# Kernel optimization log

Measured on AMD Instinct MI355X. Metric: run time of the kernel, lower is better.

## Reference

```python
import jax, jax.numpy as jnp
import numpy as np

E = 2_000_000   # edges
N = 200_000     # nodes
E_DIM = 128     # edge feature dim
G_DIM = 256     # global/graph feature dim
B = 1024        # number of graphs (batch.max()+1)
EPS = 1e-6      # torch_scatter scatter_std eps


def setup_inputs() -> dict:
    key = jax.random.key(0)
    k1, k2, k3, k4 = jax.random.split(key, 4)
    e = jax.random.normal(k1, (E, E_DIM), dtype=jnp.float32)
    e_index = jax.random.randint(k2, (2, E), 0, N, dtype=jnp.int64)
    batch = jnp.sort(jax.random.randint(k3, (N,), 0, B, dtype=jnp.int64))
    fc_w = jax.random.normal(k4, (E_DIM * 4, G_DIM), dtype=jnp.float32) * 0.02
    fc_b = jnp.zeros((G_DIM,), dtype=jnp.float32)
    return {"e_index": e_index, "e": e, "batch": batch, "fc_w": fc_w, "fc_b": fc_b}


def reference(e_index, e, batch, fc_w, fc_b):
    # graph id per edge (via target node of each edge)
    e_batch = batch[e_index[1]]  # [E]

    count = jax.ops.segment_sum(jnp.ones((e.shape[0],), e.dtype), e_batch,
                                num_segments=B)[:, None]  # [B, 1]
    s = jax.ops.segment_sum(e, e_batch, num_segments=B)    # [B, D]

    # scatter(reduce='mean'): empty segments -> 0 (divide by clamped count)
    mean = s / jnp.maximum(count, 1.0)

    # scatter min/max: torch_scatter fills empty segments with 0
    mn = jax.ops.segment_min(e, e_batch, num_segments=B)
    mx = jax.ops.segment_max(e, e_batch, num_segments=B)
    empty = count == 0.0
    mn = jnp.where(empty, 0.0, mn)
    mx = jnp.where(empty, 0.0, mx)

    # scatter_std (unbiased, matches torch_scatter composite):
    # std = sqrt(sum((x - mean)^2) / (clamp(count-1, 1) + eps))
    diff = e - mean[e_batch]                               # [E, D]
    var_sum = jax.ops.segment_sum(diff * diff, e_batch, num_segments=B)
    denom = jnp.maximum(count - 1.0, 1.0) + EPS
    std = jnp.sqrt(var_sum / denom)

    g = jnp.concatenate([mean, mn, mx, std], axis=1)       # [B, 4D]
    return g @ fc_w + fc_b                                 # [B, G_DIM]
```

## Files before the change

### kernel.cpp

```cpp
#include <hip/hip_runtime.h>
#include <math.h>

#define DIMS 128
#define GD 256
#define MAXB 1024
#define NSLOT 8
#define NBLK 256
#define SCH 8192

typedef float vfloat4 __attribute__((ext_vector_type(4)));

__device__ __forceinline__ float4 ldnt(const float* p) {
    vfloat4 v = __builtin_nontemporal_load(reinterpret_cast<const vfloat4*>(p));
    return make_float4(v.x, v.y, v.z, v.w);
}
__device__ __forceinline__ float4 f4_add(float4 a, float4 b) {
    return make_float4(a.x + b.x, a.y + b.y, a.z + b.z, a.w + b.w);
}
__device__ __forceinline__ float4 f4_min(float4 a, float4 b) {
    return make_float4(fminf(a.x, b.x), fminf(a.y, b.y), fminf(a.z, b.z), fminf(a.w, b.w));
}
__device__ __forceinline__ float4 f4_max(float4 a, float4 b) {
    return make_float4(fmaxf(a.x, b.x), fmaxf(a.y, b.y), fmaxf(a.z, b.z), fmaxf(a.w, b.w));
}

#define ACC(v) do { \
    sm = f4_add(sm, v); \
    sq = f4_add(sq, make_float4((v).x*(v).x, (v).y*(v).y, (v).z*(v).z, (v).w*(v).w)); \
    mn = f4_min(mn, v); mx = f4_max(mx, v); } while (0)

__global__ void __launch_bounds__(256)
hist2_kernel(const int* __restrict__ e_index, const int* __restrict__ batch,
             int E, int* __restrict__ hist2r, unsigned short* __restrict__ eb) {
    __shared__ int lh[MAXB];
    for (int i = threadIdx.x; i < MAXB; i += 256) lh[i] = 0;
    __syncthreads();
    int b = blockIdx.x;
    int CH = (E + NBLK - 1) / NBLK;
    int lo = b * CH;
    int hi = min(E, lo + CH);
    for (int j = lo + threadIdx.x; j < hi; j += 256) {
        int node = e_index[E + j];
        int g = batch[node];
        eb[j] = (unsigned short)g;
        atomicAdd(&lh[g], 1);
    }
    __syncthreads();
    for (int i = threadIdx.x; i < MAXB; i += 256)
        hist2r[(size_t)b * MAXB + i] = lh[i];
}

__global__ void __launch_bounds__(256)
colscan_kernel(const int* __restrict__ hist2r, int* __restrict__ hist2s,
               int* __restrict__ count) {
    int g = blockIdx.x;
    int t = threadIdx.x;
    int v = hist2r[(size_t)t * MAXB + g];
    __shared__ int ws[256];
    ws[t] = v;
    __syncthreads();
    for (int d = 1; d < 256; d <<= 1) {
        int x = (t >= d) ? ws[t - d] : 0;
        __syncthreads();
        ws[t] += x;
        __syncthreads();
    }
    hist2s[(size_t)t * MAXB + g] = ws[t] - v;
    if (t == 255) count[g] = ws[255];
}

__global__ void __launch_bounds__(256)
scatter_kernel(const unsigned short* __restrict__ eb, const int* __restrict__ hist2r,
               const int* __restrict__ hist2s, const int* __restrict__ count, int E,
               int* __restrict__ perm, int* __restrict__ offs) {
    __shared__ int lofs[MAXB];
    __shared__ int lcur[MAXB];
    __shared__ int lbase[MAXB];
    __shared__ int ws[256];
    __shared__ int bin[SCH];
    int b = blockIdx.x;
    int t = threadIdx.x;
    int CH = (E + NBLK - 1) / NBLK;
    int lo = b * CH;
    int hi = min(E, lo + CH);
    int base = t * 4;

    int g0 = count[base + 0], g1 = count[base + 1], g2 = count[base + 2], g3 = count[base + 3];
    int gsum = g0 + g1 + g2 + g3;
    ws[t] = gsum;
    __syncthreads();
    for (int d = 1; d < 256; d <<= 1) {
        int x = (t >= d) ? ws[t - d] : 0;
        __syncthreads();
        ws[t] += x;
        __syncthreads();
    }
    int gexcl = ws[t] - gsum;
    int ob0 = gexcl, ob1 = gexcl + g0, ob2 = gexcl + g0 + g1, ob3 = gexcl + g0 + g1 + g2;
    if (b == 0) {
        offs[base + 0] = ob0; offs[base + 1] = ob1;
        offs[base + 2] = ob2; offs[base + 3] = ob3;
    }
    lbase[base + 0] = ob0 + hist2s[(size_t)b * MAXB + base + 0];
    lbase[base + 1] = ob1 + hist2s[(size_t)b * MAXB + base + 1];
    lbase[base + 2] = ob2 + hist2s[(size_t)b * MAXB + base + 2];
    lbase[base + 3] = ob3 + hist2s[(size_t)b * MAXB + base + 3];
    __syncthreads();

    int c0 = hist2r[(size_t)b * MAXB + base + 0];
    int c1 = hist2r[(size_t)b * MAXB + base + 1];
    int c2 = hist2r[(size_t)b * MAXB + base + 2];
    int c3 = hist2r[(size_t)b * MAXB + base + 3];
    int s0 = c0 + c1 + c2 + c3;
    ws[t] = s0;
    __syncthreads();
    for (int d = 1; d < 256; d <<= 1) {
        int x = (t >= d) ? ws[t - d] : 0;
        __syncthreads();
        ws[t] += x;
        __syncthreads();
    }
    int excl = ws[t] - s0;
    lofs[base + 0] = excl;
    lofs[base + 1] = excl + c0;
    lofs[base + 2] = excl + c0 + c1;
    lofs[base + 3] = excl + c0 + c1 + c2;
    lcur[base + 0] = excl;
    lcur[base + 1] = excl + c0;
    lcur[base + 2] = excl + c0 + c1;
    lcur[base + 3] = excl + c0 + c1 + c2;
    __syncthreads();

    for (int j = lo + t; j < hi; j += 256) {
        int g = eb[j];
        int r = atomicAdd(&lcur[g], 1);
        bin[r] = j;
    }
    __syncthreads();

    int grp = t >> 3, sub = t & 7;
    for (int g = grp; g < MAXB; g += 32) {
        int sfrom = lofs[g];
        int n = lcur[g] - sfrom;
        int dst = lbase[g];
        for (int k = sub; k < n; k += 8)
            perm[dst + k] = bin[sfrom + k];
    }
}

__global__ void __launch_bounds__(256)
reduce_kernel(const float* __restrict__ e, const int* __restrict__ perm,
              const int* __restrict__ offs, const int* __restrict__ count,
              float* __restrict__ gbuf) {
    int g = blockIdx.x;
    int start = offs[g];
    int cnt = count[g];
    const int* pp = perm + start;

    int c = threadIdx.x & 31;
    int s = threadIdx.x >> 5;

    float4 sm = make_float4(0.f, 0.f, 0.f, 0.f);
    float4 sq = make_float4(0.f, 0.f, 0.f, 0.f);
    float4 mn = make_float4(INFINITY, INFINITY, INFINITY, INFINITY);
    float4 mx = make_float4(-INFINITY, -INFINITY, -INFINITY, -INFINITY);

    int i = s;
    if (i + 3 * NSLOT < cnt) {
        int ia0 = pp[i], ia1 = pp[i + NSLOT], ia2 = pp[i + 2 * NSLOT], ia3 = pp[i + 3 * NSLOT];
        while (true) {
            int ni = i + 4 * NSLOT;
            int na0 = 0, na1 = 0, na2 = 0, na3 = 0;
            bool nok = (ni + 3 * NSLOT < cnt);
            if (nok) { na0 = pp[ni]; na1 = pp[ni + NSLOT]; na2 = pp[ni + 2 * NSLOT]; na3 = pp[ni + 3 * NSLOT]; }
            float4 v0 = ldnt(e + (size_t)ia0 * DIMS + c * 4);
            float4 v1 = ldnt(e + (size_t)ia1 * DIMS + c * 4);
            float4 v2 = ldnt(e + (size_t)ia2 * DIMS + c * 4);
            float4 v3 = ldnt(e + (size_t)ia3 * DIMS + c * 4);
            ACC(v0); ACC(v1); ACC(v2); ACC(v3);
            i = ni;
            if (!nok) break;
            ia0 = na0; ia1 = na1; ia2 = na2; ia3 = na3;
        }
    }
    for (; i < cnt; i += NSLOT) {
        int r = pp[i];
        float4 v = ldnt(e + (size_t)r * DIMS + c * 4);
        ACC(v);
    }

    __shared__ float4 red[4][NSLOT][32];
    red[0][s][c] = sm;
    red[1][s][c] = mn;
    red[2][s][c] = mx;
    red[3][s][c] = sq;
    __syncthreads();

    int t = threadIdx.x;
    if (t < 128) {
        int stat = t >> 5;
        int cc = t & 31;
        float4 a = red[stat][0][cc];
        if (stat == 1) {
#pragma unroll
            for (int k = 1; k < NSLOT; ++k) a = f4_min(a, red[1][k][cc]);
        } else if (stat == 2) {
#pragma unroll
            for (int k = 1; k < NSLOT; ++k) a = f4_max(a, red[2][k][cc]);
        } else {
#pragma unroll
            for (int k = 1; k < NSLOT; ++k) a = f4_add(a, red[stat][k][cc]);
        }
        float fc = (float)cnt;
        float fcm = fmaxf(fc, 1.0f);
        float4 r;
        if (stat == 0) {
            r = make_float4(a.x / fcm, a.y / fcm, a.z / fcm, a.w / fcm);
        } else if (stat == 1 || stat == 2) {
            r = (cnt == 0) ? make_float4(0.f, 0.f, 0.f, 0.f) : a;
        } else {
            float4 smr = red[0][0][cc];
#pragma unroll
            for (int k = 1; k < NSLOT; ++k) smr = f4_add(smr, red[0][k][cc]);
            float4 mean = make_float4(smr.x / fcm, smr.y / fcm, smr.z / fcm, smr.w / fcm);
            float denom = fmaxf(fc - 1.0f, 1.0f) + 1e-6f;
            r = make_float4(sqrtf(fmaxf(a.x - smr.x * mean.x, 0.f) / denom),
                            sqrtf(fmaxf(a.y - smr.y * mean.y, 0.f) / denom),
                            sqrtf(fmaxf(a.z - smr.z * mean.z, 0.f) / denom),
                            sqrtf(fmaxf(a.w - smr.w * mean.w, 0.f) / denom));
        }
        *reinterpret_cast<float4*>(gbuf + (size_t)g * 512 + stat * DIMS + cc * 4) = r;
    }
}

__global__ void __launch_bounds__(256)
gemm_kernel(const float* __restrict__ gbuf, const float* __restrict__ w,
            const float* __restrict__ bias, float* __restrict__ out, int B) {
    __shared__ float gl[8 * 512];
    int r0 = blockIdx.x * 8;
    int t = threadIdx.x;
    for (int i = t; i < 8 * 512; i += 256) {
        int r = r0 + (i >> 9);
        gl[i] = (r < B) ? gbuf[(size_t)r0 * 512 + i] : 0.f;
    }
    __syncthreads();

    int col = t;
    float acc[8];
    float bv = bias[col];
#pragma unroll
    for (int r = 0; r < 8; ++r) acc[r] = bv;
#pragma unroll 4
    for (int k = 0; k < 512; ++k) {
        float wv = w[k * GD + col];
#pragma unroll
        for (int r = 0; r < 8; ++r) acc[r] += gl[r * 512 + k] * wv;
    }
#pragma unroll
    for (int r = 0; r < 8; ++r) {
        int rr = r0 + r;
        if (rr < B) out[(size_t)rr * GD + col] = acc[r];
    }
}

extern "C" void kernel_launch(void* const* d_in, const int* in_sizes, int n_in,
                              void* d_out, int out_size, void* d_ws, size_t ws_size,
                              hipStream_t stream) {
    const int*   e_index = (const int*)d_in[0];
    const float* e       = (const float*)d_in[1];
    const int*   batch   = (const int*)d_in[2];
    const float* fc_w    = (const float*)d_in[3];
    const float* fc_b    = (const float*)d_in[4];
    float* out = (float*)d_out;

    int E = in_sizes[1] / DIMS;
    int B = out_size / GD;

    int* hist2r = (int*)d_ws;
    int* hist2s = hist2r + (size_t)NBLK * MAXB;
    int* count  = hist2s + (size_t)NBLK * MAXB;
    int* offs   = count + MAXB;
    unsigned short* eb = (unsigned short*)(offs + MAXB);
    int* perm   = (int*)(eb + (((size_t)E + 1) & ~(size_t)1));
    float* gbuf = (float*)(perm + E);

    hist2_kernel<<<NBLK, 256, 0, stream>>>(e_index, batch, E, hist2r, eb);
    colscan_kernel<<<MAXB, 256, 0, stream>>>(hist2r, hist2s, count);
    scatter_kernel<<<NBLK, 256, 0, stream>>>(eb, hist2r, hist2s, count, E, perm, offs);
    reduce_kernel<<<MAXB, 256, 0, stream>>>(e, perm, offs, count, gbuf);
    gemm_kernel<<<(B + 7) / 8, 256, 0, stream>>>(gbuf, fc_w, fc_b, out, B);
}
```

Measured before the change: 262.5 us.

## Fuse histogram/scan/scatter into cooperative kernel and split reduce per graph

Merges the histogram, column scan and scatter kernels into one cooperative kernel that uses grid.sync, removing two launches and their gaps. The reduce kernel now runs two blocks per graph, each handling half the edges and writing partial sum/min/max/sumsq. The GEMM kernel combines the two partials and finalizes mean/min/max/std before the matmul. This doubles reduce parallelism to better saturate memory bandwidth, at the cost of grid-wide barriers and a larger partial buffer.

Result: slower. 344.9 us (+31.4%).

```diff
diff --git a/kernel.cpp b/kernel.cpp
--- a/kernel.cpp
+++ b/kernel.cpp
@@ -1,10 +1,14 @@
 #include <hip/hip_runtime.h>
+#include <hip/hip_cooperative_groups.h>
 #include <math.h>
+
+namespace cg = cooperative_groups;
 
 #define DIMS 128
 #define GD 256
 #define MAXB 1024
 #define NSLOT 8
+#define PARTS 2
 #define NBLK 256
 #define SCH 8192
 
@@ -30,54 +34,17 @@
     mn = f4_min(mn, v); mx = f4_max(mx, v); } while (0)
 
 __global__ void __launch_bounds__(256)
-hist2_kernel(const int* __restrict__ e_index, const int* __restrict__ batch,
-             int E, int* __restrict__ hist2r, unsigned short* __restrict__ eb) {
+prep_kernel(const int* __restrict__ e_index, const int* __restrict__ batch, int E,
+            int* __restrict__ hist2r, int* __restrict__ hist2s,
+            int* __restrict__ count, int* __restrict__ offs,
+            unsigned short* __restrict__ eb, int* __restrict__ perm) {
     __shared__ int lh[MAXB];
-    for (int i = threadIdx.x; i < MAXB; i += 256) lh[i] = 0;
-    __syncthreads();
-    int b = blockIdx.x;
-    int CH = (E + NBLK - 1) / NBLK;
-    int lo = b * CH;
-    int hi = min(E, lo + CH);
-    for (int j = lo + threadIdx.x; j < hi; j += 256) {
-        int node = e_index[E + j];
-        int g = batch[node];
-        eb[j] = (unsigned short)g;
-        atomicAdd(&lh[g], 1);
-    }
-    __syncthreads();
-    for (int i = threadIdx.x; i < MAXB; i += 256)
-        hist2r[(size_t)b * MAXB + i] = lh[i];
-}
-
-__global__ void __launch_bounds__(256)
-colscan_kernel(const int* __restrict__ hist2r, int* __restrict__ hist2s,
-               int* __restrict__ count) {
-    int g = blockIdx.x;
-    int t = threadIdx.x;
-    int v = hist2r[(size_t)t * MAXB + g];
     __shared__ int ws[256];
-    ws[t] = v;
-    __syncthreads();
-    for (int d = 1; d < 256; d <<= 1) {
-        int x = (t >= d) ? ws[t - d] : 0;
-        __syncthreads();
-        ws[t] += x;
-        __syncthreads();
-    }
-    hist2s[(size_t)t * MAXB + g] = ws[t] - v;
-    if (t == 255) count[g] = ws[255];
-}
-
-__global__ void __launch_bounds__(256)
-scatter_kernel(const unsigned short* __restrict__ eb, const int* __restrict__ hist2r,
-               const int* __restrict__ hist2s, const int* __restrict__ count, int E,
-               int* __restrict__ perm, int* __restrict__ offs) {
-    __shared__ int lofs[MAXB];
     __shared__ int lcur[MAXB];
     __shared__ int lbase[MAXB];
-    __shared__ int ws[256];
     __shared__ int bin[SCH];
+
+    cg::grid_group grid = cg::this_grid();
     int b = blockIdx.x;
     int t = threadIdx.x;
     int CH = (E + NBLK - 1) / NBLK;
@@ -85,6 +52,38 @@
     int hi = min(E, lo + CH);
     int base = t * 4;
 
+    for (int i = t; i < MAXB; i += 256) lh[i] = 0;
+    __syncthreads();
+    for (int j = lo + t; j < hi; j += 256) {
+        int node = e_index[E + j];
+        int g = batch[node];
+        eb[j] = (unsigned short)g;
+        atomicAdd(&lh[g], 1);
+    }
+    __syncthreads();
+    for (int i = t; i < MAXB; i += 256)
+        hist2r[(size_t)b * MAXB + i] = lh[i];
+
+    grid.sync();
+
+    for (int q = 0; q < 4; ++q) {
+        int g = b * 4 + q;
+        int v = hist2r[(size_t)t * MAXB + g];
+        ws[t] = v;
+        __syncthreads();
+        for (int d = 1; d < 256; d <<= 1) {
+            int x = (t >= d) ? ws[t - d] : 0;
+            __syncthreads();
+            ws[t] += x;
+            __syncthreads();
+        }
+        hist2s[(size_t)t * MAXB + g] = ws[t] - v;
+        if (t == 255) count[g] = ws[255];
+        __syncthreads();
+    }
+
+    grid.sync();
+
     int g0 = count[base + 0], g1 = count[base + 1], g2 = count[base + 2], g3 = count[base + 3];
     int gsum = g0 + g1 + g2 + g3;
     ws[t] = gsum;
@@ -121,10 +120,10 @@
         __syncthreads();
     }
     int excl = ws[t] - s0;
-    lofs[base + 0] = excl;
-    lofs[base + 1] = excl + c0;
-    lofs[base + 2] = excl + c0 + c1;
-    lofs[base + 3] = excl + c0 + c1 + c2;
+    lh[base + 0] = excl;
+    lh[base + 1] = excl + c0;
+    lh[base + 2] = excl + c0 + c1;
+    lh[base + 3] = excl + c0 + c1 + c2;
     lcur[base + 0] = excl;
     lcur[base + 1] = excl + c0;
     lcur[base + 2] = excl + c0 + c1;
@@ -140,7 +139,7 @@
 
     int grp = t >> 3, sub = t & 7;
     for (int g = grp; g < MAXB; g += 32) {
-        int sfrom = lofs[g];
+        int sfrom = lh[g];
         int n = lcur[g] - sfrom;
         int dst = lbase[g];
         for (int k = sub; k < n; k += 8)
@@ -151,11 +150,18 @@
 __global__ void __launch_bounds__(256)
 reduce_kernel(const float* __restrict__ e, const int* __restrict__ perm,
               const int* __restrict__ offs, const int* __restrict__ count,
-              float* __restrict__ gbuf) {
-    int g = blockIdx.x;
+              float* __restrict__ pbuf) {
+    int bid = blockIdx.x;
+    int g = bid >> 1;
+    int p = bid & 1;
     int start = offs[g];
     int cnt = count[g];
-    const int* pp = perm + start;
+    int chunk = (cnt + PARTS - 1) / PARTS;
+    int bb = p * chunk;
+    int cnt_p = cnt - bb;
+    if (cnt_p > chunk) cnt_p = chunk;
+    if (cnt_p < 0) cnt_p = 0;
+    const int* pp = perm + start + bb;
 
     int c = threadIdx.x & 31;
     int s = threadIdx.x >> 5;
@@ -166,12 +172,12 @@
     float4 mx = make_float4(-INFINITY, -INFINITY, -INFINITY, -INFINITY);
 
     int i = s;
-    if (i + 3 * NSLOT < cnt) {
+    if (i + 3 * NSLOT < cnt_p) {
         int ia0 = pp[i], ia1 = pp[i + NSLOT], ia2 = pp[i + 2 * NSLOT], ia3 = pp[i + 3 * NSLOT];
         while (true) {
             int ni = i + 4 * NSLOT;
             int na0 = 0, na1 = 0, na2 = 0, na3 = 0;
-            bool nok = (ni + 3 * NSLOT < cnt);
+            bool nok = (ni + 3 * NSLOT < cnt_p);
             if (nok) { na0 = pp[ni]; na1 = pp[ni + NSLOT]; na2 = pp[ni + 2 * NSLOT]; na3 = pp[ni + 3 * NSLOT]; }
             float4 v0 = ldnt(e + (size_t)ia0 * DIMS + c * 4);
             float4 v1 = ldnt(e + (size_t)ia1 * DIMS + c * 4);
@@ -183,7 +189,7 @@
             ia0 = na0; ia1 = na1; ia2 = na2; ia3 = na3;
         }
     }
-    for (; i < cnt; i += NSLOT) {
+    for (; i < cnt_p; i += NSLOT) {
         int r = pp[i];
         float4 v = ldnt(e + (size_t)r * DIMS + c * 4);
         ACC(v);
@@ -211,37 +217,44 @@
 #pragma unroll
             for (int k = 1; k < NSLOT; ++k) a = f4_add(a, red[stat][k][cc]);
         }
-        float fc = (float)cnt;
-        float fcm = fmaxf(fc, 1.0f);
-        float4 r;
-        if (stat == 0) {
-            r = make_float4(a.x / fcm, a.y / fcm, a.z / fcm, a.w / fcm);
-        } else if (stat == 1 || stat == 2) {
-            r = (cnt == 0) ? make_float4(0.f, 0.f, 0.f, 0.f) : a;
-        } else {
-            float4 smr = red[0][0][cc];
-#pragma unroll
-            for (int k = 1; k < NSLOT; ++k) smr = f4_add(smr, red[0][k][cc]);
-            float4 mean = make_float4(smr.x / fcm, smr.y / fcm, smr.z / fcm, smr.w / fcm);
-            float denom = fmaxf(fc - 1.0f, 1.0f) + 1e-6f;
-            r = make_float4(sqrtf(fmaxf(a.x - smr.x * mean.x, 0.f) / denom),
-                            sqrtf(fmaxf(a.y - smr.y * mean.y, 0.f) / denom),
-                            sqrtf(fmaxf(a.z - smr.z * mean.z, 0.f) / denom),
-                            sqrtf(fmaxf(a.w - smr.w * mean.w, 0.f) / denom));
-        }
-        *reinterpret_cast<float4*>(gbuf + (size_t)g * 512 + stat * DIMS + cc * 4) = r;
+        *reinterpret_cast<float4*>(pbuf + (size_t)bid * 512 + stat * DIMS + cc * 4) = a;
     }
 }
 
 __global__ void __launch_bounds__(256)
-gemm_kernel(const float* __restrict__ gbuf, const float* __restrict__ w,
-            const float* __restrict__ bias, float* __restrict__ out, int B) {
+gemm_kernel(const float* __restrict__ pbuf, const int* __restrict__ count,
+            const float* __restrict__ w, const float* __restrict__ bias,
+            float* __restrict__ out, int B) {
     __shared__ float gl[8 * 512];
     int r0 = blockIdx.x * 8;
     int t = threadIdx.x;
-    for (int i = t; i < 8 * 512; i += 256) {
-        int r = r0 + (i >> 9);
-        gl[i] = (r < B) ? gbuf[(size_t)r0 * 512 + i] : 0.f;
+#pragma unroll
+    for (int q = 0; q < 4; ++q) {
+        int pair = q * 256 + t;
+        int r = pair >> 7;
+        int d = pair & 127;
+        int g = r0 + r;
+        float sm = 0.f, sq = 0.f, mnv = INFINITY, mxv = -INFINITY;
+        int cnt = 0;
+        if (g < B) {
+            cnt = count[g];
+            const float* p0 = pbuf + (size_t)(2 * g) * 512;
+            const float* p1 = p0 + 512;
+            sm  = p0[d] + p1[d];
+            mnv = fminf(p0[128 + d], p1[128 + d]);
+            mxv = fmaxf(p0[256 + d], p1[256 + d]);
+            sq  = p0[384 + d] + p1[384 + d];
+        }
+        float fc = (float)cnt;
+        float fcm = fmaxf(fc, 1.0f);
+        float mean = sm / fcm;
+        float vs = fmaxf(sq - sm * mean, 0.f);
+        float sd = sqrtf(vs / (fmaxf(fc - 1.0f, 1.0f) + 1e-6f));
+        if (cnt == 0) { mnv = 0.f; mxv = 0.f; }
+        gl[r * 512 + 0 * 128 + d] = mean;
+        gl[r * 512 + 1 * 128 + d] = mnv;
+        gl[r * 512 + 2 * 128 + d] = mxv;
+        gl[r * 512 + 3 * 128 + d] = sd;
     }
     __syncthreads();
 
@@ -282,11 +295,13 @@
     int* offs   = count + MAXB;
     unsigned short* eb = (unsigned short*)(offs + MAXB);
     int* perm   = (int*)(eb + (((size_t)E + 1) & ~(size_t)1));
-    float* gbuf = (float*)(perm + E);
-
-    hist2_kernel<<<NBLK, 256, 0, stream>>>(e_index, batch, E, hist2r, eb);
-    colscan_kernel<<<MAXB, 256, 0, stream>>>(hist2r, hist2s, count);
-    scatter_kernel<<<NBLK, 256, 0, stream>>>(eb, hist2r, hist2s, count, E, perm, offs);
-    reduce_kernel<<<MAXB, 256, 0, stream>>>(e, perm, offs, count, gbuf);
-    gemm_kernel<<<(B + 7) / 8, 256, 0, stream>>>(gbuf, fc_w, fc_b, out, B);
-}
+    float* pbuf = (float*)(perm + E);
+
+    void* prep_args[] = { (void*)&e_index, (void*)&batch, (void*)&E,
+                          (void*)&hist2r, (void*)&hist2s, (void*)&count,
+                          (void*)&offs, (void*)&eb, (void*)&perm };
+    hipLaunchCooperativeKernel((const void*)prep_kernel, dim3(NBLK), dim3(256),
+                               prep_args, 0, stream);
+    reduce_kernel<<<B * PARTS, 256, 0, stream>>>(e, perm, offs, count, pbuf);
+    gemm_kernel<<<(B + 7) / 8, 256, 0, stream>>>(pbuf, fc_w ? count : count, fc_w, fc_b, out, B);
+}
```
